# Optimization experiments

Measured on AMD Instinct MI355X. Metric: run time of the kernel, lower is better.

Reference implementation:

```python
import jax, jax.numpy as jnp
import numpy as np

B, S, L, H, C = 16, 2048, 256, 768, 512

def setup_inputs() -> dict:
    key = jax.random.key(0)
    ks = jax.random.split(key, 9)
    sc = 1.0 / np.sqrt(H)
    return {
        "input_hidden_states": jax.random.normal(ks[0], (B, S, H), jnp.float32),
        "label_hidden_states": jax.random.normal(ks[1], (L, H), jnp.float32),
        "Wi": jax.random.normal(ks[2], (C, H), jnp.float32) * sc,
        "bi": jnp.zeros((C,), jnp.float32),
        "Wl": jax.random.normal(ks[3], (C, H), jnp.float32) * sc,
        "bl": jnp.zeros((C,), jnp.float32),
        "Wia": jax.random.normal(ks[4], (C, H), jnp.float32) * sc,
        "bia": jnp.zeros((C,), jnp.float32),
        "Wla": jax.random.normal(ks[5], (C, H), jnp.float32) * sc,
        "bla": jnp.zeros((C,), jnp.float32),
        "context": jax.random.uniform(ks[6], (C,), jnp.float32),
        "Wp": jax.random.normal(ks[7], (H, C), jnp.float32) * (1.0 / np.sqrt(C)),
    }

def reference(input_hidden_states, label_hidden_states, Wi, bi, Wl, bl,
              Wia, bia, Wla, bla, context, Wp):
    # Dropout is identity in eval mode.
    x = input_hidden_states            # [B,S,H]
    lab = label_hidden_states          # [L,H] (original repeats over batch; math is identical)
    input_trans = jax.nn.sigmoid(jnp.einsum('bsh,ch->bsc', x, Wi) + bi)      # [B,S,C]
    label_trans = jax.nn.sigmoid(lab @ Wl.T + bl)                            # [L,C]
    input_attn = jax.nn.sigmoid(jnp.einsum('bsh,ch->bsc', x, Wia) + bia)    # [B,S,C]
    label_attn = jax.nn.sigmoid(lab @ Wla.T + bla)                          # [L,C]
    # attn logits: (context * input_attn) @ label_attn^T  -> [B,S,L]
    logits = jnp.einsum('bsc,lc->bsl', input_attn * context, label_attn)
    attn = jax.nn.softmax(logits, axis=-1)                                   # [B,S,L]
    # trilinear reduction: sum_{s,l} input_trans[b,s,c] * attn[b,s,l] * label_trans[l,c]
    weighted = jnp.einsum('bsl,lc->bsc', attn, label_trans)                  # [B,S,C]
    fusion = jnp.sum(input_trans * weighted, axis=1)                         # [B,C]
    return fusion @ Wp.T                                                     # [B,H]
```

## Files before the change

### kernel.cpp

```cpp
#include <hip/hip_runtime.h>

#define H_DIM 768
#define C_DIM 512
#define L_DIM 256
#define S_DIM 2048
#define B_DIM 16

#define IA_STRIDE 520
#define ATTN_STRIDE 264

typedef __attribute__((ext_vector_type(8))) short short8;
typedef __attribute__((ext_vector_type(4))) float f32x4;
typedef __attribute__((ext_vector_type(2))) __fp16 half2v;

#define MFMA_F16(a, b, c) __builtin_amdgcn_mfma_f32_16x16x32_f16((a), (b), (c), 0, 0, 0)

__device__ __forceinline__ unsigned short f2h(float f) {
    _Float16 h = (_Float16)f;
    return __builtin_bit_cast(unsigned short, h);
}
__device__ __forceinline__ float h2f(unsigned short u) {
    _Float16 h = __builtin_bit_cast(_Float16, u);
    return (float)h;
}
__device__ __forceinline__ float sigmoid_f(float x) { return 1.0f / (1.0f + __expf(-x)); }

__device__ __forceinline__ short8 cvt8(const float* p) {
    const float4* q = (const float4*)(const void*)p;
    float4 u = q[0], v = q[1];
    half2v h0 = __builtin_amdgcn_cvt_pkrtz(u.x, u.y);
    half2v h1 = __builtin_amdgcn_cvt_pkrtz(u.z, u.w);
    half2v h2 = __builtin_amdgcn_cvt_pkrtz(v.x, v.y);
    half2v h3 = __builtin_amdgcn_cvt_pkrtz(v.z, v.w);
    int4 pk = { __builtin_bit_cast(int, h0), __builtin_bit_cast(int, h1),
                __builtin_bit_cast(int, h2), __builtin_bit_cast(int, h3) };
    return __builtin_bit_cast(short8, pk);
}


__global__ __launch_bounds__(256) void prep_w(
    const float* __restrict__ Wi, const float* __restrict__ Wia,
    const float* __restrict__ Wl, const float* __restrict__ Wla,
    unsigned short* __restrict__ Wi_f, unsigned short* __restrict__ Wia_f,
    unsigned short* __restrict__ Wl_f, unsigned short* __restrict__ Wla_f)
{
    const int tid = blockIdx.x * 256 + threadIdx.x;
    const int m   = tid / 49152;
    const int idx = tid - m * 49152;
    const int ct   = idx / 1536;
    const int rem  = idx - ct * 1536;
    const int kt   = rem >> 6;
    const int lane = rem & 63;
    const int row  = ct * 16 + (lane & 15);
    const int kcol = kt * 32 + (lane >> 4) * 8;
    const float* src = (m == 0 ? Wi : (m == 1 ? Wia : (m == 2 ? Wl : Wla)));
    unsigned short* dst = (m == 0 ? Wi_f : (m == 1 ? Wia_f : (m == 2 ? Wl_f : Wla_f)));
    short8 v = cvt8(src + (size_t)row * H_DIM + kcol);
    const int frag = ((ct >> 3) * 24 + kt) * 8 + (ct & 7);
    *(short8*)(void*)(dst + ((size_t)frag * 64 + lane) * 8) = v;
}

__global__ __launch_bounds__(256) void prep_x(
    const float* __restrict__ x, unsigned short* __restrict__ x_f)
{
    const int tid = blockIdx.x * 256 + threadIdx.x;
    const int mt  = tid / 1536;
    const int rem = tid - mt * 1536;
    const int kt  = rem >> 6;
    const int lane = rem & 63;
    const int row = mt * 16 + (lane & 15);
    const int col = kt * 32 + (lane >> 4) * 8;
    short8 v = cvt8(x + (size_t)row * H_DIM + col);
    *(short8*)(void*)(x_f + ((size_t)(mt * 24 + kt) * 64 + lane) * 8) = v;
}

__global__ __launch_bounds__(256) void label_mfma(
    const float* __restrict__ lab,
    const unsigned short* __restrict__ Wl_f,  const float* __restrict__ bl,
    const unsigned short* __restrict__ Wla_f, const float* __restrict__ bla,
    const float* __restrict__ ctx,
    unsigned short* __restrict__ la_f,
    unsigned short* __restrict__ lt_f)
{
    const int tid  = threadIdx.x;
    const int wave = tid >> 6;
    const int lane = tid & 63;
    const int quad = lane >> 4;
    const int c16  = lane & 15;
    const int ct2  = blockIdx.x & 7;
    const int mh   = blockIdx.x >> 3;
    const int ct   = ct2 * 4 + wave;
    const int n0   = ct * 16;
    const int l0   = mh * 32;

    const f32x4 z4 = {0.f, 0.f, 0.f, 0.f};
    f32x4 a1[2], a2[2];
#pragma unroll
    for (int mt = 0; mt < 2; ++mt) { a1[mt] = z4; a2[mt] = z4; }

    const float* lb = lab + (size_t)(l0 + c16) * H_DIM + quad * 8;
    const short8* wl8  = (const short8*)(const void*)Wl_f  + ((size_t)(ct >> 3) * 24 * 8 + (ct & 7)) * 64 + lane;
    const short8* wla8 = (const short8*)(const void*)Wla_f + ((size_t)(ct >> 3) * 24 * 8 + (ct & 7)) * 64 + lane;
    for (int kt = 0; kt < 24; ++kt) {
        short8 b1 = wl8[kt * 8 * 64];
        short8 b2 = wla8[kt * 8 * 64];
#pragma unroll
        for (int mt = 0; mt < 2; ++mt) {
            short8 a = cvt8(lb + mt * 16 * H_DIM + kt * 32);
            a1[mt] = MFMA_F16(a, b1, a1[mt]);
            a2[mt] = MFMA_F16(a, b2, a2[mt]);
        }
    }
    const int c = n0 + c16;
    const float blv = bl[c], blav = bla[c], cv = ctx[c];
#pragma unroll
    for (int mt = 0; mt < 2; ++mt)
#pragma unroll
        for (int r = 0; r < 4; ++r) {
            const int l = l0 + mt * 16 + quad * 4 + r;
            const float ltv = sigmoid_f(a1[mt][r] + blv);
            const float lav = sigmoid_f(a2[mt][r] + blav) * cv;
            {
                const int ctc = c >> 4, ktl = l >> 5;
                const int frag = ((ctc >> 3) * 8 + ktl) * 8 + (ctc & 7);
                const int ln = (c & 15) | (((l >> 3) & 3) << 4);
                lt_f[((size_t)frag * 64 + ln) * 8 + (l & 7)] = f2h(ltv);
            }
            {
                const int lt = l >> 4, ktc = c >> 5;
                const int frag = ((lt >> 2) * 16 + ktc) * 4 + (lt & 3);
                const int ln = (l & 15) | (((c >> 3) & 3) << 4);
                la_f[((size_t)frag * 64 + ln) * 8 + (c & 7)] = f2h(lav);
            }
        }
}

template<bool XF>
__global__ __launch_bounds__(256, 4) void fused_main(
    const unsigned short* __restrict__ x_f,
    const float* __restrict__ x,
    const float* __restrict__ bi,
    const float* __restrict__ bia,
    const unsigned short* __restrict__ Wi_f,
    const unsigned short* __restrict__ Wia_f,
    const unsigned short* __restrict__ lt_f,
    const unsigned short* __restrict__ la_f,
    float* __restrict__ fusion)
{
    __shared__ unsigned short lds_buf[32 * IA_STRIDE];
    __shared__ float rowscratch[4 * 32];
    __shared__ float inv_lds[32];

    const int tid  = threadIdx.x;
    const int wave = tid >> 6;
    const int lane = tid & 63;
    const int quad = lane >> 4;
    const int c16  = lane & 15;

    const int row0 = blockIdx.x * 32;
    const int b    = row0 >> 11;

    const f32x4 z4 = {0.f, 0.f, 0.f, 0.f};
    const int n0 = wave * 128;

    const float*  xb  = x + (size_t)(row0 + c16) * H_DIM + quad * 8;
    const short8* xf8 = (const short8*)(const void*)x_f + ((size_t)blockIdx.x * 2 * 24) * 64 + lane;

    {
        f32x4 acc[2][8];
#pragma unroll
        for (int mt = 0; mt < 2; ++mt)
#pragma unroll
            for (int nt = 0; nt < 8; ++nt) acc[mt][nt] = z4;
        const short8* wa8 = (const short8*)(const void*)Wia_f + (size_t)wave * 192 * 64 + lane;
        for (int kt = 0; kt < 24; ++kt) {
            short8 a0, a1;
            if constexpr (XF) { a0 = xf8[kt * 64]; a1 = xf8[(24 + kt) * 64]; }
            else { a0 = cvt8(xb + kt * 32); a1 = cvt8(xb + 16 * H_DIM + kt * 32); }
#pragma unroll
            for (int nt = 0; nt < 8; ++nt) {
                short8 ba = wa8[(kt * 8 + nt) * 64];
                acc[0][nt] = MFMA_F16(a0, ba, acc[0][nt]);
                acc[1][nt] = MFMA_F16(a1, ba, acc[1][nt]);
            }
        }
#pragma unroll
        for (int nt = 0; nt < 8; ++nt) {
            const int col = n0 + nt * 16 + c16;
            const float bv = bia[col];
#pragma unroll
            for (int mt = 0; mt < 2; ++mt)
#pragma unroll
                for (int r = 0; r < 4; ++r) {
                    const int row = mt * 16 + quad * 4 + r;
                    lds_buf[row * IA_STRIDE + col] = f2h(sigmoid_f(acc[mt][nt][r] + bv));
                }
        }
    }
    __syncthreads();

    const int n0l = wave * 64;
    f32x4 accl[2][4];
#pragma unroll
    for (int mt = 0; mt < 2; ++mt)
#pragma unroll
        for (int nt = 0; nt < 4; ++nt) accl[mt][nt] = z4;
    {
        const unsigned short* ab = lds_buf + c16 * IA_STRIDE + quad * 8;
        const short8* la8 = (const short8*)(const void*)la_f + (size_t)wave * 64 * 64 + lane;
        for (int kt = 0; kt < 16; ++kt) {
            const int kk = kt * 32;
            short8 a0 = *(const short8*)(const void*)(ab + kk);
            short8 a1 = *(const short8*)(const void*)(ab + 16 * IA_STRIDE + kk);
#pragma unroll
            for (int nt = 0; nt < 4; ++nt) {
                short8 bfr = la8[(kt * 4 + nt) * 64];
                accl[0][nt] = MFMA_F16(a0, bfr, accl[0][nt]);
                accl[1][nt] = MFMA_F16(a1, bfr, accl[1][nt]);
            }
        }
    }
    __syncthreads();

    float rmax[2][4];
#pragma unroll
    for (int mt = 0; mt < 2; ++mt)
#pragma unroll
        for (int r = 0; r < 4; ++r) {
            float m = accl[mt][0][r];
#pragma unroll
            for (int nt = 1; nt < 4; ++nt) m = fmaxf(m, accl[mt][nt][r]);
#pragma unroll
            for (int off = 1; off < 16; off <<= 1) m = fmaxf(m, __shfl_xor(m, off, 64));
            rmax[mt][r] = m;
        }
    if (c16 == 0) {
#pragma unroll
        for (int mt = 0; mt < 2; ++mt)
#pragma unroll
            for (int r = 0; r < 4; ++r)
                rowscratch[wave * 32 + mt * 16 + quad * 4 + r] = rmax[mt][r];
    }
    __syncthreads();
    float rsum[2][4];
#pragma unroll
    for (int mt = 0; mt < 2; ++mt)
#pragma unroll
        for (int r = 0; r < 4; ++r) {
            const int row = mt * 16 + quad * 4 + r;
            float gm = rowscratch[row];
#pragma unroll
            for (int w = 1; w < 4; ++w) gm = fmaxf(gm, rowscratch[w * 32 + row]);
            float s = 0.f;
#pragma unroll
            for (int nt = 0; nt < 4; ++nt) {
                float e = __expf(accl[mt][nt][r] - gm);
                accl[mt][nt][r] = e;
                s += e;
            }
#pragma unroll
            for (int off = 1; off < 16; off <<= 1) s += __shfl_xor(s, off, 64);
            rsum[mt][r] = s;
        }
    __syncthreads();
    if (c16 == 0) {
#pragma unroll
        for (int mt = 0; mt < 2; ++mt)
#pragma unroll
            for (int r = 0; r < 4; ++r)
                rowscratch[wave * 32 + mt * 16 + quad * 4 + r] = rsum[mt][r];
    }
    __syncthreads();
#pragma unroll
    for (int mt = 0; mt < 2; ++mt)
#pragma unroll
        for (int r = 0; r < 4; ++r) {
            const int row = mt * 16 + quad * 4 + r;
            const float st = rowscratch[row] + rowscratch[32 + row]
                           + rowscratch[64 + row] + rowscratch[96 + row];
            if (wave == 0 && c16 == 0) inv_lds[row] = 1.0f / st;
#pragma unroll
            for (int nt = 0; nt < 4; ++nt)
                lds_buf[row * ATTN_STRIDE + n0l + nt * 16 + c16] = f2h(accl[mt][nt][r]);
        }
    __syncthreads();

    f32x4 accw[2][8];
#pragma unroll
    for (int mt = 0; mt < 2; ++mt)
#pragma unroll
        for (int nt = 0; nt < 8; ++nt) accw[mt][nt] = z4;
    {
        const unsigned short* ab = lds_buf + c16 * ATTN_STRIDE + quad * 8;
        const short8* lt8 = (const short8*)(const void*)lt_f + (size_t)wave * 64 * 64 + lane;
        for (int kt = 0; kt < 8; ++kt) {
            const int kk = kt * 32;
            short8 a0 = *(const short8*)(const void*)(ab + kk);
            short8 a1 = *(const short8*)(const void*)(ab + 16 * ATTN_STRIDE + kk);
#pragma unroll
            for (int nt = 0; nt < 8; ++nt) {
                short8 bfr = lt8[(kt * 8 + nt) * 64];
                accw[0][nt] = MFMA_F16(a0, bfr, accw[0][nt]);
                accw[1][nt] = MFMA_F16(a1, bfr, accw[1][nt]);
            }
        }
    }
    __syncthreads();

    {
        float invr[2][4];
#pragma unroll
        for (int mt = 0; mt < 2; ++mt)
#pragma unroll
            for (int r = 0; r < 4; ++r) invr[mt][r] = inv_lds[mt * 16 + quad * 4 + r];
#pragma unroll
        for (int nt = 0; nt < 8; ++nt) {
            const int col = n0 + nt * 16 + c16;
#pragma unroll
            for (int mt = 0; mt < 2; ++mt)
#pragma unroll
                for (int r = 0; r < 4; ++r) {
                    const int row = mt * 16 + quad * 4 + r;
                    lds_buf[row * IA_STRIDE + col] = f2h(accw[mt][nt][r] * invr[mt][r]);
                }
        }
    }

    {
        f32x4 acc[2][8];
#pragma unroll
        for (int mt = 0; mt < 2; ++mt)
#pragma unroll
            for (int nt = 0; nt < 8; ++nt) acc[mt][nt] = z4;
        const short8* wi8 = (const short8*)(const void*)Wi_f + (size_t)wave * 192 * 64 + lane;
        for (int kt = 0; kt < 24; ++kt) {
            short8 a0, a1;
            if constexpr (XF) { a0 = xf8[kt * 64]; a1 = xf8[(24 + kt) * 64]; }
            else { a0 = cvt8(xb + kt * 32); a1 = cvt8(xb + 16 * H_DIM + kt * 32); }
#pragma unroll
            for (int nt = 0; nt < 8; ++nt) {
                short8 bw = wi8[(kt * 8 + nt) * 64];
                acc[0][nt] = MFMA_F16(a0, bw, acc[0][nt]);
                acc[1][nt] = MFMA_F16(a1, bw, acc[1][nt]);
            }
        }
#pragma unroll
        for (int nt = 0; nt < 8; ++nt) {
            const int col = n0 + nt * 16 + c16;
            const float bv = bi[col];
            float s = 0.f;
#pragma unroll
            for (int mt = 0; mt < 2; ++mt)
#pragma unroll
                for (int r = 0; r < 4; ++r) {
                    const int row = mt * 16 + quad * 4 + r;
                    s += h2f(lds_buf[row * IA_STRIDE + col]) * sigmoid_f(acc[mt][nt][r] + bv);
                }
            s += __shfl_xor(s, 16, 64);
            s += __shfl_xor(s, 32, 64);
            if (lane < 16) atomicAdd(&fusion[b * C_DIM + col], s);
        }
    }
}

__global__ __launch_bounds__(256) void out_kernel(
    const float* __restrict__ fusion,
    const float* __restrict__ Wp,
    float* __restrict__ out)
{
    const int idx = blockIdx.x * 256 + threadIdx.x;
    const int R   = idx >> 3;
    const int sub = idx & 7;
    const int bb  = R / H_DIM;
    const int h   = R - bb * H_DIM;
    const float* wp = Wp + (size_t)h * C_DIM;
    const float* f  = fusion + bb * C_DIM;
    float s = 0.f;
#pragma unroll
    for (int j = 0; j < 16; ++j) {
        const int c = j * 32 + sub * 4;
        float4 wv = *(const float4*)(const void*)(wp + c);
        float4 fv = *(const float4*)(const void*)(f + c);
        s += fv.x * wv.x + fv.y * wv.y + fv.z * wv.z + fv.w * wv.w;
    }
    s += __shfl_xor(s, 1, 64);
    s += __shfl_xor(s, 2, 64);
    s += __shfl_xor(s, 4, 64);
    if (sub == 0) out[R] = s;
}

extern "C" void kernel_launch(void* const* d_in, const int* in_sizes, int n_in,
                              void* d_out, int out_size, void* d_ws, size_t ws_size,
                              hipStream_t stream)
{
    const float* x    = (const float*)d_in[0];
    const float* lab  = (const float*)d_in[1];
    const float* Wi   = (const float*)d_in[2];
    const float* bi   = (const float*)d_in[3];
    const float* Wl   = (const float*)d_in[4];
    const float* bl   = (const float*)d_in[5];
    const float* Wia  = (const float*)d_in[6];
    const float* bia  = (const float*)d_in[7];
    const float* Wla  = (const float*)d_in[8];
    const float* bla  = (const float*)d_in[9];
    const float* ctx  = (const float*)d_in[10];
    const float* Wp   = (const float*)d_in[11];

    char* ws = (char*)d_ws;
    unsigned short* Wi_f  = (unsigned short*)(ws);
    unsigned short* Wia_f = (unsigned short*)(ws + 786432);
    unsigned short* Wl_f  = (unsigned short*)(ws + 1572864);
    unsigned short* Wla_f = (unsigned short*)(ws + 2359296);
    unsigned short* la_f  = (unsigned short*)(ws + 3145728);
    unsigned short* lt_f  = (unsigned short*)(ws + 3407872);
    float* fusion         = (float*)(ws + 3670016);
    unsigned short* x_f   = (unsigned short*)(ws + 3702784);
    const size_t NEED_XF  = 3702784 + (size_t)32768 * 768 * 2;

    (void)hipMemsetAsync(fusion, 0, B_DIM * C_DIM * sizeof(float), stream);
    prep_w<<<768, 256, 0, stream>>>(Wi, Wia, Wl, Wla, Wi_f, Wia_f, Wl_f, Wla_f);
    label_mfma<<<64, 256, 0, stream>>>(lab, Wl_f, bl, Wla_f, bla, ctx, la_f, lt_f);
    if (ws_size >= NEED_XF) {
        prep_x<<<12288, 256, 0, stream>>>(x, x_f);
        fused_main<true><<<(B_DIM * S_DIM) / 32, 256, 0, stream>>>(
            x_f, x, bi, bia, Wi_f, Wia_f, lt_f, la_f, fusion);
    } else {
        fused_main<false><<<(B_DIM * S_DIM) / 32, 256, 0, stream>>>(
            nullptr, x, bi, bia, Wi_f, Wia_f, lt_f, la_f, fusion);
    }
    out_kernel<<<384, 256, 0, stream>>>(fusion, Wp, (float*)d_out);
}
```

Before: 332.8 us.

## Double fused-kernel row tile to 64 with 8 waves and coalesce prep_x via LDS

Result: faster. 293.8 us (-11.7%).

```diff
diff --git a/kernel.cpp b/kernel.cpp
--- a/kernel.cpp
+++ b/kernel.cpp
@@ -8,6 +8,7 @@
 
 #define IA_STRIDE 520
 #define ATTN_STRIDE 264
+#define XP_STRIDE 776
 
 typedef __attribute__((ext_vector_type(8))) short short8;
 typedef __attribute__((ext_vector_type(4))) float f32x4;
@@ -63,15 +64,32 @@
 __global__ __launch_bounds__(256) void prep_x(
     const float* __restrict__ x, unsigned short* __restrict__ x_f)
 {
-    const int tid = blockIdx.x * 256 + threadIdx.x;
-    const int mt  = tid / 1536;
-    const int rem = tid - mt * 1536;
-    const int kt  = rem >> 6;
-    const int lane = rem & 63;
-    const int row = mt * 16 + (lane & 15);
-    const int col = kt * 32 + (lane >> 4) * 8;
-    short8 v = cvt8(x + (size_t)row * H_DIM + col);
-    *(short8*)(void*)(x_f + ((size_t)(mt * 24 + kt) * 64 + lane) * 8) = v;
+    __shared__ unsigned short tile[16 * XP_STRIDE];
+    const int t  = threadIdx.x;
+    const int mt = blockIdx.x;
+    const float4* src = (const float4*)(const void*)(x + (size_t)mt * 16 * H_DIM);
+#pragma unroll
+    for (int i = 0; i < 12; ++i) {
+        const int id  = i * 256 + t;
+        const int row = id / 192;
+        const int c4  = id - row * 192;
+        float4 v = src[id];
+        half2v h0 = __builtin_amdgcn_cvt_pkrtz(v.x, v.y);
+        half2v h1 = __builtin_amdgcn_cvt_pkrtz(v.z, v.w);
+        uint2 pk = { __builtin_bit_cast(unsigned int, h0),
+                     __builtin_bit_cast(unsigned int, h1) };
+        *(uint2*)(void*)(tile + row * XP_STRIDE + c4 * 4) = pk;
+    }
+    __syncthreads();
+    const int lane = t & 63;
+    const int wave = t >> 6;
+#pragma unroll
+    for (int q = 0; q < 6; ++q) {
+        const int kt = wave * 6 + q;
+        short8 v = *(const short8*)(const void*)(
+            tile + (lane & 15) * XP_STRIDE + kt * 32 + (lane >> 4) * 8);
+        *(short8*)(void*)(x_f + ((size_t)(mt * 24 + kt) * 64 + lane) * 8) = v;
+    }
 }
 
 __global__ __launch_bounds__(256) void label_mfma(
@@ -136,7 +154,7 @@
 }
 
 template<bool XF>
-__global__ __launch_bounds__(256, 4) void fused_main(
+__global__ __launch_bounds__(512, 4) void fused_main(
     const unsigned short* __restrict__ x_f,
     const float* __restrict__ x,
     const float* __restrict__ bi,
@@ -147,9 +165,9 @@
     const unsigned short* __restrict__ la_f,
     float* __restrict__ fusion)
 {
-    __shared__ unsigned short lds_buf[32 * IA_STRIDE];
-    __shared__ float rowscratch[4 * 32];
-    __shared__ float inv_lds[32];
+    __shared__ unsigned short lds_buf[64 * IA_STRIDE];
+    __shared__ float rowscratch[8 * 64];
+    __shared__ float inv_lds[64];
 
     const int tid  = threadIdx.x;
     const int wave = tid >> 6;
@@ -157,204 +175,228 @@
     const int quad = lane >> 4;
     const int c16  = lane & 15;
 
-    const int row0 = blockIdx.x * 32;
+    const int row0 = blockIdx.x * 64;
     const int b    = row0 >> 11;
 
     const f32x4 z4 = {0.f, 0.f, 0.f, 0.f};
-    const int n0 = wave * 128;
+    const int n0 = wave * 64;
 
     const float*  xb  = x + (size_t)(row0 + c16) * H_DIM + quad * 8;
-    const short8* xf8 = (const short8*)(const void*)x_f + ((size_t)blockIdx.x * 2 * 24) * 64 + lane;
+    const short8* xf8 = (const short8*)(const void*)x_f + (size_t)blockIdx.x * 96 * 64 + lane;
+    const size_t wofs = ((size_t)(wave >> 1) * 192 + (size_t)(wave & 1) * 4) * 64 + lane;
 
     {
-        f32x4 acc[2][8];
-#pragma unroll
-        for (int mt = 0; mt < 2; ++mt)
-#pragma unroll
-            for (int nt = 0; nt < 8; ++nt) acc[mt][nt] = z4;
-        const short8* wa8 = (const short8*)(const void*)Wia_f + (size_t)wave * 192 * 64 + lane;
+        f32x4 acc[4][4];
+#pragma unroll
+        for (int m = 0; m < 4; ++m)
+#pragma unroll
+            for (int nt = 0; nt < 4; ++nt) acc[m][nt] = z4;
+        const short8* wa8 = (const short8*)(const void*)Wia_f + wofs;
         for (int kt = 0; kt < 24; ++kt) {
-            short8 a0, a1;
-            if constexpr (XF) { a0 = xf8[kt * 64]; a1 = xf8[(24 + kt) * 64]; }
-            else { a0 = cvt8(xb + kt * 32); a1 = cvt8(xb + 16 * H_DIM + kt * 32); }
-#pragma unroll
-            for (int nt = 0; nt < 8; ++nt) {
-                short8 ba = wa8[(kt * 8 + nt) * 64];
-                acc[0][nt] = MFMA_F16(a0, ba, acc[0][nt]);
-                acc[1][nt] = MFMA_F16(a1, ba, acc[1][nt]);
-            }
-        }
-#pragma unroll
-        for (int nt = 0; nt < 8; ++nt) {
+            short8 a0, a1, a2, a3;
+            if constexpr (XF) {
+                a0 = xf8[kt * 64];        a1 = xf8[(24 + kt) * 64];
+                a2 = xf8[(48 + kt) * 64]; a3 = xf8[(72 + kt) * 64];
+            } else {
+                a0 = cvt8(xb + kt * 32);                a1 = cvt8(xb + 16 * H_DIM + kt * 32);
+                a2 = cvt8(xb + 32 * H_DIM + kt * 32);   a3 = cvt8(xb + 48 * H_DIM + kt * 32);
+            }
+#pragma unroll
+            for (int nt = 0; nt < 4; ++nt) {
+                short8 bw = wa8[(kt * 8 + nt) * 64];
+                acc[0][nt] = MFMA_F16(a0, bw, acc[0][nt]);
+                acc[1][nt] = MFMA_F16(a1, bw, acc[1][nt]);
+                acc[2][nt] = MFMA_F16(a2, bw, acc[2][nt]);
+                acc[3][nt] = MFMA_F16(a3, bw, acc[3][nt]);
+            }
+        }
+#pragma unroll
+        for (int nt = 0; nt < 4; ++nt) {
             const int col = n0 + nt * 16 + c16;
             const float bv = bia[col];
 #pragma unroll
-            for (int mt = 0; mt < 2; ++mt)
+            for (int m = 0; m < 4; ++m)
 #pragma unroll
                 for (int r = 0; r < 4; ++r) {
-                    const int row = mt * 16 + quad * 4 + r;
-                    lds_buf[row * IA_STRIDE + col] = f2h(sigmoid_f(acc[mt][nt][r] + bv));
+                    const int row = m * 16 + quad * 4 + r;
+                    lds_buf[row * IA_STRIDE + col] = f2h(sigmoid_f(acc[m][nt][r] + bv));
                 }
         }
     }
     __syncthreads();
 
-    const int n0l = wave * 64;
-    f32x4 accl[2][4];
-#pragma unroll
-    for (int mt = 0; mt < 2; ++mt)
-#pragma unroll
-        for (int nt = 0; nt < 4; ++nt) accl[mt][nt] = z4;
+    const int n0l = wave * 32;
+    f32x4 accl[4][2];
+#pragma unroll
+    for (int m = 0; m < 4; ++m)
+#pragma unroll
+        for (int j = 0; j < 2; ++j) accl[m][j] = z4;
     {
         const unsigned short* ab = lds_buf + c16 * IA_STRIDE + quad * 8;
-        const short8* la8 = (const short8*)(const void*)la_f + (size_t)wave * 64 * 64 + lane;
+        const short8* la8 = (const short8*)(const void*)la_f
+                          + ((size_t)(wave >> 1) * 64 + (size_t)(wave & 1) * 2) * 64 + lane;
         for (int kt = 0; kt < 16; ++kt) {
             const int kk = kt * 32;
             short8 a0 = *(const short8*)(const void*)(ab + kk);
             short8 a1 = *(const short8*)(const void*)(ab + 16 * IA_STRIDE + kk);
-#pragma unroll
-            for (int nt = 0; nt < 4; ++nt) {
-                short8 bfr = la8[(kt * 4 + nt) * 64];
-                accl[0][nt] = MFMA_F16(a0, bfr, accl[0][nt]);
-                accl[1][nt] = MFMA_F16(a1, bfr, accl[1][nt]);
-            }
-        }
-    }
-    __syncthreads();
-
-    float rmax[2][4];
-#pragma unroll
-    for (int mt = 0; mt < 2; ++mt)
+            short8 a2 = *(const short8*)(const void*)(ab + 32 * IA_STRIDE + kk);
+            short8 a3 = *(const short8*)(const void*)(ab + 48 * IA_STRIDE + kk);
+#pragma unroll
+            for (int j = 0; j < 2; ++j) {
+                short8 bfr = la8[(kt * 4 + j) * 64];
+                accl[0][j] = MFMA_F16(a0, bfr, accl[0][j]);
+                accl[1][j] = MFMA_F16(a1, bfr, accl[1][j]);
+                accl[2][j] = MFMA_F16(a2, bfr, accl[2][j]);
+                accl[3][j] = MFMA_F16(a3, bfr, accl[3][j]);
+            }
+        }
+    }
+    __syncthreads();
+
+    float rmax[4][4];
+#pragma unroll
+    for (int m = 0; m < 4; ++m)
 #pragma unroll
         for (int r = 0; r < 4; ++r) {
-            float m = accl[mt][0][r];
-#pragma unroll
-            for (int nt = 1; nt < 4; ++nt) m = fmaxf(m, accl[mt][nt][r]);
-#pragma unroll
-            for (int off = 1; off < 16; off <<= 1) m = fmaxf(m, __shfl_xor(m, off, 64));
-            rmax[mt][r] = m;
+            float mx = fmaxf(accl[m][0][r], accl[m][1][r]);
+#pragma unroll
+            for (int off = 1; off < 16; off <<= 1) mx = fmaxf(mx, __shfl_xor(mx, off, 64));
+            rmax[m][r] = mx;
         }
     if (c16 == 0) {
 #pragma unroll
-        for (int mt = 0; mt < 2; ++mt)
+        for (int m = 0; m < 4; ++m)
 #pragma unroll
             for (int r = 0; r < 4; ++r)
-                rowscratch[wave * 32 + mt * 16 + quad * 4 + r] = rmax[mt][r];
-    }
-    __syncthreads();
-    float rsum[2][4];
-#pragma unroll
-    for (int mt = 0; mt < 2; ++mt)
+                rowscratch[wave * 64 + m * 16 + quad * 4 + r] = rmax[m][r];
+    }
+    __syncthreads();
+    float rsum[4][4];
+#pragma unroll
+    for (int m = 0; m < 4; ++m)
 #pragma unroll
         for (int r = 0; r < 4; ++r) {
-            const int row = mt * 16 + quad * 4 + r;
+            const int row = m * 16 + quad * 4 + r;
             float gm = rowscratch[row];
 #pragma unroll
-            for (int w = 1; w < 4; ++w) gm = fmaxf(gm, rowscratch[w * 32 + row]);
+            for (int w = 1; w < 8; ++w) gm = fmaxf(gm, rowscratch[w * 64 + row]);
             float s = 0.f;
 #pragma unroll
-            for (int nt = 0; nt < 4; ++nt) {
-                float e = __expf(accl[mt][nt][r] - gm);
-                accl[mt][nt][r] = e;
+            for (int j = 0; j < 2; ++j) {
+                float e = __expf(accl[m][j][r] - gm);
+                accl[m][j][r] = e;
                 s += e;
             }
 #pragma unroll
             for (int off = 1; off < 16; off <<= 1) s += __shfl_xor(s, off, 64);
-            rsum[mt][r] = s;
+            rsum[m][r] = s;
         }
     __syncthreads();
     if (c16 == 0) {
 #pragma unroll
-        for (int mt = 0; mt < 2; ++mt)
+        for (int m = 0; m < 4; ++m)
 #pragma unroll
             for (int r = 0; r < 4; ++r)
-                rowscratch[wave * 32 + mt * 16 + quad * 4 + r] = rsum[mt][r];
-    }
-    __syncthreads();
-#pragma unroll
-    for (int mt = 0; mt < 2; ++mt)
+                rowscratch[wave * 64 + m * 16 + quad * 4 + r] = rsum[m][r];
+    }
+    __syncthreads();
+#pragma unroll
+    for (int m = 0; m < 4; ++m)
 #pragma unroll
         for (int r = 0; r < 4; ++r) {
-            const int row = mt * 16 + quad * 4 + r;
-            const float st = rowscratch[row] + rowscratch[32 + row]
-                           + rowscratch[64 + row] + rowscratch[96 + row];
+            const int row = m * 16 + quad * 4 + r;
+            float st = 0.f;
+#pragma unroll
+            for (int w = 0; w < 8; ++w) st += rowscratch[w * 64 + row];
             if (wave == 0 && c16 == 0) inv_lds[row] = 1.0f / st;
 #pragma unroll
-            for (int nt = 0; nt < 4; ++nt)
-                lds_buf[row * ATTN_STRIDE + n0l + nt * 16 + c16] = f2h(accl[mt][nt][r]);
-        }
-    __syncthreads();
-
-    f32x4 accw[2][8];
-#pragma unroll
-    for (int mt = 0; mt < 2; ++mt)
-#pragma unroll
-        for (int nt = 0; nt < 8; ++nt) accw[mt][nt] = z4;
+            for (int j = 0; j < 2; ++j)
+                lds_buf[row * ATTN_STRIDE + n0l + j * 16 + c16] = f2h(accl[m][j][r]);
+        }
+    __syncthreads();
+
+    f32x4 accw[4][4];
+#pragma unroll
+    for (int m = 0; m < 4; ++m)
+#pragma unroll
+        for (int nt = 0; nt < 4; ++nt) accw[m][nt] = z4;
     {
         const unsigned short* ab = lds_buf + c16 * ATTN_STRIDE + quad * 8;
-        const short8* lt8 = (const short8*)(const void*)lt_f + (size_t)wave * 64 * 64 + lane;
+        const short8* lt8 = (const short8*)(const void*)lt_f
+                          + ((size_t)(wave >> 1) * 64 + (size_t)(wave & 1) * 4) * 64 + lane;
         for (int kt = 0; kt < 8; ++kt) {
             const int kk = kt * 32;
             short8 a0 = *(const short8*)(const void*)(ab + kk);
             short8 a1 = *(const short8*)(const void*)(ab + 16 * ATTN_STRIDE + kk);
-#pragma unroll
-            for (int nt = 0; nt < 8; ++nt) {
+            short8 a2 = *(const short8*)(const void*)(ab + 32 * ATTN_STRIDE + kk);
+            short8 a3 = *(const short8*)(const void*)(ab + 48 * ATTN_STRIDE + kk);
+#pragma unroll
+            for (int nt = 0; nt < 4; ++nt) {
                 short8 bfr = lt8[(kt * 8 + nt) * 64];
                 accw[0][nt] = MFMA_F16(a0, bfr, accw[0][nt]);
                 accw[1][nt] = MFMA_F16(a1, bfr, accw[1][nt]);
+                accw[2][nt] = MFMA_F16(a2, bfr, accw[2][nt]);
+                accw[3][nt] = MFMA_F16(a3, bfr, accw[3][nt]);
             }
         }
     }
     __syncthreads();
 
     {
-        float invr[2][4];
-#pragma unroll
-        for (int mt = 0; mt < 2; ++mt)
-#pragma unroll
-            for (int r = 0; r < 4; ++r) invr[mt][r] = inv_lds[mt * 16 + quad * 4 + r];
-#pragma unroll
-        for (int nt = 0; nt < 8; ++nt) {
+        float invr[4][4];
+#pragma unroll
+        for (int m = 0; m < 4; ++m)
+#pragma unroll
+            for (int r = 0; r < 4; ++r) invr[m][r] = inv_lds[m * 16 + quad * 4 + r];
+#pragma unroll
+        for (int nt = 0; nt < 4; ++nt) {
             const int col = n0 + nt * 16 + c16;
 #pragma unroll
-            for (int mt = 0; mt < 2; ++mt)
+            for (int m = 0; m < 4; ++m)
 #pragma unroll
                 for (int r = 0; r < 4; ++r) {
-                    const int row = mt * 16 + quad * 4 + r;
-                    lds_buf[row * IA_STRIDE + col] = f2h(accw[mt][nt][r] * invr[mt][r]);
+                    const int row = m * 16 + quad * 4 + r;
+                    lds_buf[row * IA_STRIDE + col] = f2h(accw[m][nt][r] * invr[m][r]);
                 }
         }
     }
 
     {
-        f32x4 acc[2][8];
-#pragma unroll
-        for (int mt = 0; mt < 2; ++mt)
-#pragma unroll
-            for (int nt = 0; nt < 8; ++nt) acc[mt][nt] = z4;
-        const short8* wi8 = (const short8*)(const void*)Wi_f + (size_t)wave * 192 * 64 + lane;
+        f32x4 acc[4][4];
+#pragma unroll
+        for (int m = 0; m < 4; ++m)
+#pragma unroll
+            for (int nt = 0; nt < 4; ++nt) acc[m][nt] = z4;
+        const short8* wi8 = (const short8*)(const void*)Wi_f + wofs;
         for (int kt = 0; kt < 24; ++kt) {
-            short8 a0, a1;
-            if constexpr (XF) { a0 = xf8[kt * 64]; a1 = xf8[(24 + kt) * 64]; }
-            else { a0 = cvt8(xb + kt * 32); a1 = cvt8(xb + 16 * H_DIM + kt * 32); }
-#pragma unroll
-            for (int nt = 0; nt < 8; ++nt) {
+            short8 a0, a1, a2, a3;
+            if constexpr (XF) {
+                a0 = xf8[kt * 64];        a1 = xf8[(24 + kt) * 64];
+                a2 = xf8[(48 + kt) * 64]; a3 = xf8[(72 + kt) * 64];
+            } else {
+                a0 = cvt8(xb + kt * 32);                a1 = cvt8(xb + 16 * H_DIM + kt * 32);
+                a2 = cvt8(xb + 32 * H_DIM + kt * 32);   a3 = cvt8(xb + 48 * H_DIM + kt * 32);
+            }
+#pragma unroll
+            for (int nt = 0; nt < 4; ++nt) {
                 short8 bw = wi8[(kt * 8 + nt) * 64];
                 acc[0][nt] = MFMA_F16(a0, bw, acc[0][nt]);
                 acc[1][nt] = MFMA_F16(a1, bw, acc[1][nt]);
-            }
-        }
-#pragma unroll
-        for (int nt = 0; nt < 8; ++nt) {
+                acc[2][nt] = MFMA_F16(a2, bw, acc[2][nt]);
+                acc[3][nt] = MFMA_F16(a3, bw, acc[3][nt]);
+            }
+        }
+#pragma unroll
+        for (int nt = 0; nt < 4; ++nt) {
             const int col = n0 + nt * 16 + c16;
             const float bv = bi[col];
             float s = 0.f;
 #pragma unroll
-            for (int mt = 0; mt < 2; ++mt)
+            for (int m = 0; m < 4; ++m)
 #pragma unroll
                 for (int r = 0; r < 4; ++r) {
-                    const int row = mt * 16 + quad * 4 + r;
-                    s += h2f(lds_buf[row * IA_STRIDE + col]) * sigmoid_f(acc[mt][nt][r] + bv);
+                    const int row = m * 16 + quad * 4 + r;
+                    s += h2f(lds_buf[row * IA_STRIDE + col]) * sigmoid_f(acc[m][nt][r] + bv);
                 }
             s += __shfl_xor(s, 16, 64);
             s += __shfl_xor(s, 32, 64);
@@ -421,11 +463,11 @@
     prep_w<<<768, 256, 0, stream>>>(Wi, Wia, Wl, Wla, Wi_f, Wia_f, Wl_f, Wla_f);
     label_mfma<<<64, 256, 0, stream>>>(lab, Wl_f, bl, Wla_f, bla, ctx, la_f, lt_f);
     if (ws_size >= NEED_XF) {
-        prep_x<<<12288, 256, 0, stream>>>(x, x_f);
-        fused_main<true><<<(B_DIM * S_DIM) / 32, 256, 0, stream>>>(
+        prep_x<<<2048, 256, 0, stream>>>(x, x_f);
+        fused_main<true><<<(B_DIM * S_DIM) / 64, 512, 0, stream>>>(
             x_f, x, bi, bia, Wi_f, Wia_f, lt_f, la_f, fusion);
     } else {
-        fused_main<false><<<(B_DIM * S_DIM) / 32, 256, 0, stream>>>(
+        fused_main<false><<<(B_DIM * S_DIM) / 64, 512, 0, stream>>>(
             nullptr, x, bi, bia, Wi_f, Wia_f, lt_f, la_f, fusion);
     }
     out_kernel<<<384, 256, 0, stream>>>(fusion, Wp, (float*)d_out);
```
